# Optimization experiments

Hardware: AMD Instinct MI355X
Metric: run time of the kernel (lower is better)

## Reference

```python
import jax, jax.numpy as jnp
import numpy as np

N_VOX = 200000   # active voxels
K = 27           # 3x3x3 kernel offsets
P = 100000       # rulebook pairs per kernel offset
C_IN = 64
C_OUT = 64
BN_EPS = 1e-5


def setup_inputs() -> dict:
    key = jax.random.key(0)
    k1, k2, k3, k4, k5 = jax.random.split(key, 5)
    features = jax.random.normal(k1, (N_VOX, C_IN), dtype=jnp.float32)
    weight = jax.random.normal(k2, (K, C_IN, C_OUT), dtype=jnp.float32) * 0.05
    bias = jax.random.normal(k3, (C_OUT,), dtype=jnp.float32) * 0.05
    gamma = jnp.ones((C_OUT,), dtype=jnp.float32)
    beta = jnp.zeros((C_OUT,), dtype=jnp.float32)
    in_idx = jax.random.randint(k4, (K, P), 0, N_VOX, dtype=jnp.int32)
    out_idx = jax.random.randint(k5, (K, P), 0, N_VOX, dtype=jnp.int32)
    return {"features": features, "weight": weight, "bias": bias,
            "gamma": gamma, "beta": beta, "in_idx": in_idx, "out_idx": out_idx}


def reference(features, weight, bias, gamma, beta, in_idx, out_idx):
    # --- sparse submanifold conv: gather -> per-offset GEMM -> scatter-add ---
    gathered = features[in_idx]                         # [K, P, C_in]
    partial = jnp.einsum('kpc,kcd->kpd', gathered, weight)  # [K, P, C_out]
    out = jnp.zeros((N_VOX, C_OUT), dtype=features.dtype)
    out = out.at[out_idx.reshape(-1)].add(partial.reshape(-1, C_OUT))
    out = out + bias                                    # conv bias
    # --- BatchNorm1d (training mode: batch stats, biased variance) ---
    mean = jnp.mean(out, axis=0)
    var = jnp.mean(jnp.square(out - mean), axis=0)
    normed = (out - mean) * jax.lax.rsqrt(var + BN_EPS) * gamma + beta
    # --- ReLU ---
    return jnp.maximum(normed, 0.0)
```

## Files before the change

kernel.cpp:

```cpp
#include <hip/hip_runtime.h>
#include <hip/hip_bf16.h>

#define N_VOX 200000
#define KOFF 27
#define PPK 100000
#define C 64
#define BN_EPS 1e-5f

typedef __bf16 bf16x8 __attribute__((ext_vector_type(8)));
typedef __bf16 bf16x4 __attribute__((ext_vector_type(4)));
typedef float f32x4 __attribute__((ext_vector_type(4)));

__global__ __launch_bounds__(256)
void convert_features(const float* __restrict__ f, __bf16* __restrict__ fb)
{
    const size_t total4 = (size_t)N_VOX * C / 4;
    const size_t i = (size_t)blockIdx.x * blockDim.x + threadIdx.x;
    if (i >= total4) return;
    const float4 v = ((const float4*)f)[i];
    bf16x4 o;
    o.x = (__bf16)v.x; o.y = (__bf16)v.y; o.z = (__bf16)v.z; o.w = (__bf16)v.w;
    ((bf16x4*)fb)[i] = o;
}

__global__ __launch_bounds__(256)
void convert_weight(const float* __restrict__ w, __bf16* __restrict__ wt)
{
    const int k = blockIdx.x;
    const float* W = w + (size_t)k * C * C;
    __bf16* Wt = wt + (size_t)k * C * C;
    for (int idx = threadIdx.x; idx < C * C; idx += 256) {
        const int ci = idx >> 6, co = idx & 63;
        Wt[co * C + ci] = (__bf16)W[idx];
    }
}

__global__ __launch_bounds__(256)
void conv_mfma(const __bf16* __restrict__ featb, const __bf16* __restrict__ wtb,
               const int* __restrict__ in_idx, const int* __restrict__ out_idx,
               float* __restrict__ out)
{
    constexpr int TP = 256;
    constexpr int STRIDE = 72;
    __shared__ __bf16 sA[TP * STRIDE];
    __shared__ int s_out[TP];

    const int k = blockIdx.y;
    const int tile_base = blockIdx.x * TP;
    const int t = threadIdx.x;
    const int lane = t & 63;
    const int wave = t >> 6;
    const int m16 = lane & 15;
    const int quad = lane >> 4;

    const __bf16* Wt = wtb + (size_t)k * C * C;
    bf16x8 bfrag[4][2];
#pragma unroll
    for (int nt = 0; nt < 4; ++nt)
#pragma unroll
        for (int kc = 0; kc < 2; ++kc)
            bfrag[nt][kc] = *(const bf16x8*)(Wt + (nt * 16 + m16) * C + kc * 32 + quad * 8);

    {
        const int pair = tile_base + t;
        s_out[t] = (pair < PPK) ? out_idx[(size_t)k * PPK + pair] : 0;
    }

    const int c8 = t & 7;
    const int r0 = t >> 3;
#pragma unroll
    for (int it = 0; it < 8; ++it) {
        const int r = r0 + it * 32;
        const int pair = tile_base + r;
        const int row = (pair < PPK) ? in_idx[(size_t)k * PPK + pair] : 0;
        const float4 v = *(const float4*)(featb + (size_t)row * C + c8 * 8);
        *(float4*)(sA + r * STRIDE + c8 * 8) = v;
    }
    __syncthreads();

    f32x4 acc[4][4] = {};
    const int mbase = wave * 64;
#pragma unroll
    for (int kc = 0; kc < 2; ++kc) {
        bf16x8 afrag[4];
#pragma unroll
        for (int mt = 0; mt < 4; ++mt)
            afrag[mt] = *(const bf16x8*)(sA + (mbase + mt * 16 + m16) * STRIDE + kc * 32 + quad * 8);
#pragma unroll
        for (int nt = 0; nt < 4; ++nt)
#pragma unroll
            for (int mt = 0; mt < 4; ++mt)
                acc[mt][nt] = __builtin_amdgcn_mfma_f32_16x16x32_bf16(
                    afrag[mt], bfrag[nt][kc], acc[mt][nt], 0, 0, 0);
    }

#pragma unroll
    for (int mt = 0; mt < 4; ++mt) {
#pragma unroll
        for (int reg = 0; reg < 4; ++reg) {
            const int r = mbase + mt * 16 + quad * 4 + reg;
            const int pair = tile_base + r;
            if (pair < PPK) {
                const int o = s_out[r];
                float* orow = out + (size_t)o * C + m16;
#pragma unroll
                for (int nt = 0; nt < 4; ++nt)
                    unsafeAtomicAdd(orow + nt * 16, acc[mt][nt][reg]);
            }
        }
    }
}

__global__ __launch_bounds__(256)
void stats_kernel(const float* __restrict__ out,
                  float* __restrict__ stats,
                  int rows_per_block)
{
    __shared__ float ssum[256];
    __shared__ float ssq[256];
    const int c   = threadIdx.x & 63;
    const int sub = threadIdx.x >> 6;
    const int row0 = blockIdx.x * rows_per_block;
    const int row1 = min(row0 + rows_per_block, N_VOX);
    float s = 0.f, q = 0.f;
    for (int r = row0 + sub; r < row1; r += 4) {
        const float v = out[(size_t)r * C + c];
        s += v;
        q += v * v;
    }
    ssum[threadIdx.x] = s;
    ssq[threadIdx.x]  = q;
    __syncthreads();
    if (sub == 0) {
        s = ssum[c] + ssum[64 + c] + ssum[128 + c] + ssum[192 + c];
        q = ssq[c]  + ssq[64 + c]  + ssq[128 + c]  + ssq[192 + c];
        unsafeAtomicAdd(&stats[c], s);
        unsafeAtomicAdd(&stats[64 + c], q);
    }
}

__global__ void finalize_params(const float* __restrict__ stats,
                                const float* __restrict__ gamma,
                                const float* __restrict__ beta,
                                float* __restrict__ ss)
{
    const int c = threadIdx.x;
    const float inv_n = 1.0f / (float)N_VOX;
    const float mean  = stats[c] * inv_n;
    const float var   = stats[64 + c] * inv_n - mean * mean;
    const float scale = rsqrtf(var + BN_EPS) * gamma[c];
    ss[c]      = scale;
    ss[64 + c] = beta[c] - mean * scale;
}

__global__ __launch_bounds__(256)
void norm_kernel(float* __restrict__ out, const float* __restrict__ ss)
{
    const size_t total4 = (size_t)N_VOX * C / 4;
    const size_t idx = (size_t)blockIdx.x * blockDim.x + threadIdx.x;
    if (idx >= total4) return;
    const int c4 = (int)(idx & 15);
    float4 v = ((const float4*)out)[idx];
    const float4 sc = ((const float4*)ss)[c4];
    const float4 sh = ((const float4*)(ss + 64))[c4];
    v.x = fmaxf(v.x * sc.x + sh.x, 0.f);
    v.y = fmaxf(v.y * sc.y + sh.y, 0.f);
    v.z = fmaxf(v.z * sc.z + sh.z, 0.f);
    v.w = fmaxf(v.w * sc.w + sh.w, 0.f);
    ((float4*)out)[idx] = v;
}

extern "C" void kernel_launch(void* const* d_in, const int* in_sizes, int n_in,
                              void* d_out, int out_size, void* d_ws, size_t ws_size,
                              hipStream_t stream)
{
    const float* features = (const float*)d_in[0];
    const float* weight   = (const float*)d_in[1];
    const float* gamma    = (const float*)d_in[3];
    const float* beta     = (const float*)d_in[4];
    const int*   in_idx   = (const int*)d_in[5];
    const int*   out_idx  = (const int*)d_in[6];
    float* out = (float*)d_out;

    __bf16* featb = (__bf16*)d_ws;
    __bf16* wtb   = featb + (size_t)N_VOX * C;
    float*  stats = (float*)(wtb + (size_t)KOFF * C * C);
    float*  ss    = stats + 128;

    hipMemsetAsync(out, 0, (size_t)N_VOX * C * sizeof(float), stream);
    hipMemsetAsync(stats, 0, 128 * sizeof(float), stream);

    const size_t total4 = (size_t)N_VOX * C / 4;
    convert_features<<<(int)((total4 + 255) / 256), 256, 0, stream>>>(features, featb);
    convert_weight<<<KOFF, 256, 0, stream>>>(weight, wtb);

    dim3 cgrid((PPK + 255) / 256, KOFF);
    conv_mfma<<<cgrid, 256, 0, stream>>>(featb, wtb, in_idx, out_idx, out);

    const int rpb = (N_VOX + 511) / 512;
    stats_kernel<<<512, 256, 0, stream>>>(out, stats, rpb);

    finalize_params<<<1, 64, 0, stream>>>(stats, gamma, beta, ss);

    norm_kernel<<<(int)((total4 + 255) / 256), 256, 0, stream>>>(out, ss);
}
```

Baseline: 735.5 us.

## Replace float atomic scatter with counting-sort bucketed partials and segmented reduction

Builds a per-output-voxel histogram and prefix scan, then the conv kernel writes each pair's bf16 partial row into a slot grouped by destination voxel instead of doing float atomics into the output. A reduce kernel then sums each voxel's contiguous segment, writes the output and accumulates the BN statistics in the same pass. This removes the output memset, the 27×100k×64 scattered float atomics and the separate stats pass. In exchange it adds several small kernels, about 345 MB of bf16 partial traffic, and rounds partials to bf16 before summation. It falls back to the atomic path when the workspace is too small.

After: 736.2 us. Within noise of the previous version (+0.1%).

```diff
diff --git a/kernel.cpp b/kernel.cpp
--- a/kernel.cpp
+++ b/kernel.cpp
@@ -4,6 +4,7 @@
 #define N_VOX 200000
 #define KOFF 27
 #define PPK 100000
+#define NPAIRS (KOFF * PPK)
 #define C 64
 #define BN_EPS 1e-5f
 
@@ -36,14 +37,84 @@
 }
 
 __global__ __launch_bounds__(256)
-void conv_mfma(const __bf16* __restrict__ featb, const __bf16* __restrict__ wtb,
-               const int* __restrict__ in_idx, const int* __restrict__ out_idx,
-               float* __restrict__ out)
+void hist_kernel(const int* __restrict__ out_idx, int* __restrict__ cnt)
+{
+    const int i = blockIdx.x * 256 + threadIdx.x;
+    if (i < NPAIRS) atomicAdd(&cnt[out_idx[i]], 1);
+}
+
+__global__ __launch_bounds__(256)
+void scan_block_sums(const int* __restrict__ cnt, int* __restrict__ bsum)
+{
+    __shared__ int s[256];
+    const int t = threadIdx.x;
+    const int i0 = blockIdx.x * 1024 + t * 4;
+    int v = 0;
+#pragma unroll
+    for (int j = 0; j < 4; ++j) { const int i = i0 + j; if (i < N_VOX) v += cnt[i]; }
+    s[t] = v;
+    __syncthreads();
+    for (int d = 128; d > 0; d >>= 1) {
+        if (t < d) s[t] += s[t + d];
+        __syncthreads();
+    }
+    if (t == 0) bsum[blockIdx.x] = s[0];
+}
+
+__global__ __launch_bounds__(256)
+void scan_base(const int* __restrict__ bsum, int* __restrict__ bbase, int nblk)
+{
+    __shared__ int s[256];
+    const int t = threadIdx.x;
+    const int v = (t < nblk) ? bsum[t] : 0;
+    s[t] = v;
+    for (int d = 1; d < 256; d <<= 1) {
+        __syncthreads();
+        const int x = (t >= d) ? s[t - d] : 0;
+        __syncthreads();
+        s[t] += x;
+    }
+    if (t < nblk) bbase[t] = s[t] - v;
+}
+
+__global__ __launch_bounds__(256)
+void scan_write(const int* __restrict__ cnt, const int* __restrict__ bbase,
+                int* __restrict__ offs, int* __restrict__ cursor)
+{
+    __shared__ int s[256];
+    const int t = threadIdx.x;
+    const int i0 = blockIdx.x * 1024 + t * 4;
+    int v[4]; int local = 0;
+#pragma unroll
+    for (int j = 0; j < 4; ++j) {
+        const int i = i0 + j;
+        v[j] = (i < N_VOX) ? cnt[i] : 0;
+        local += v[j];
+    }
+    s[t] = local;
+    for (int d = 1; d < 256; d <<= 1) {
+        __syncthreads();
+        const int x = (t >= d) ? s[t - d] : 0;
+        __syncthreads();
+        s[t] += x;
+    }
+    int run = s[t] - local + bbase[blockIdx.x];
+#pragma unroll
+    for (int j = 0; j < 4; ++j) {
+        const int i = i0 + j;
+        if (i < N_VOX) { offs[i] = run; cursor[i] = run; run += v[j]; }
+    }
+}
+
+__global__ __launch_bounds__(256)
+void conv_mfma_sorted(const __bf16* __restrict__ featb, const __bf16* __restrict__ wtb,
+                      const int* __restrict__ in_idx, const int* __restrict__ out_idx,
+                      int* __restrict__ cursor, __bf16* __restrict__ partial)
 {
     constexpr int TP = 256;
     constexpr int STRIDE = 72;
     __shared__ __bf16 sA[TP * STRIDE];
-    __shared__ int s_out[TP];
+    __shared__ int s_dest[TP];
 
     const int k = blockIdx.y;
     const int tile_base = blockIdx.x * TP;
@@ -63,7 +134,10 @@
 
     {
         const int pair = tile_base + t;
-        s_out[t] = (pair < PPK) ? out_idx[(size_t)k * PPK + pair] : 0;
+        if (pair < PPK) {
+            const int ov = out_idx[(size_t)k * PPK + pair];
+            s_dest[t] = atomicAdd(&cursor[ov], 1);
+        }
     }
 
     const int c8 = t & 7;
@@ -93,47 +167,160 @@
                 acc[mt][nt] = __builtin_amdgcn_mfma_f32_16x16x32_bf16(
                     afrag[mt], bfrag[nt][kc], acc[mt][nt], 0, 0, 0);
     }
-
-#pragma unroll
-    for (int mt = 0; mt < 4; ++mt) {
+    __syncthreads();
+
+#pragma unroll
+    for (int mt = 0; mt < 4; ++mt)
+#pragma unroll
+        for (int reg = 0; reg < 4; ++reg) {
+            const int r = mbase + mt * 16 + quad * 4 + reg;
+#pragma unroll
+            for (int nt = 0; nt < 4; ++nt)
+                sA[r * STRIDE + nt * 16 + m16] = (__bf16)acc[mt][nt][reg];
+        }
+    __syncthreads();
+
+    const int hw = t >> 5;
+    const int l2 = t & 31;
+    for (int r = hw; r < TP; r += 8) {
+        const int pair = tile_base + r;
+        if (pair < PPK) {
+            const unsigned v = *(const unsigned*)((const char*)sA + (size_t)r * STRIDE * 2 + l2 * 4);
+            *(unsigned*)((char*)partial + (size_t)s_dest[r] * 128 + l2 * 4) = v;
+        }
+    }
+}
+
+__global__ __launch_bounds__(256)
+void reduce_stats(const __bf16* __restrict__ partial, const int* __restrict__ offs,
+                  float* __restrict__ out, float* __restrict__ stats)
+{
+    __shared__ float ssum[256];
+    __shared__ float ssq[256];
+    const int t = threadIdx.x;
+    const int lane = t & 63;
+    const int wave = t >> 6;
+    const int wglobal = blockIdx.x * 4 + wave;
+    const int nw = gridDim.x * 4;
+    const unsigned short* P = (const unsigned short*)partial;
+    float s = 0.f, q = 0.f;
+    for (int v = wglobal; v < N_VOX; v += nw) {
+        const int b = offs[v];
+        const int e = (v == N_VOX - 1) ? NPAIRS : offs[v + 1];
+        float a0 = 0.f, a1 = 0.f;
+        int i = b;
+        for (; i + 1 < e; i += 2) {
+            const unsigned u0 = P[(size_t)i * 64 + lane];
+            const unsigned u1 = P[(size_t)(i + 1) * 64 + lane];
+            a0 += __uint_as_float(u0 << 16);
+            a1 += __uint_as_float(u1 << 16);
+        }
+        if (i < e) a0 += __uint_as_float((unsigned)P[(size_t)i * 64 + lane] << 16);
+        const float a = a0 + a1;
+        out[(size_t)v * 64 + lane] = a;
+        s += a;
+        q += a * a;
+    }
+    ssum[t] = s;
+    ssq[t] = q;
+    __syncthreads();
+    if (wave == 0) {
+        s = ssum[lane] + ssum[64 + lane] + ssum[128 + lane] + ssum[192 + lane];
+        q = ssq[lane] + ssq[64 + lane] + ssq[128 + lane] + ssq[192 + lane];
+        unsafeAtomicAdd(&stats[lane], s);
+        unsafeAtomicAdd(&stats[64 + lane], q);
+    }
+}
+
+__global__ __launch_bounds__(256)
+void conv_mfma_atomic(const __bf16* __restrict__ featb, const __bf16* __restrict__ wtb,
+                      const int* __restrict__ in_idx, const int* __restrict__ out_idx,
+                      float* __restrict__ out)
+{
+    constexpr int TP = 256;
+    constexpr int STRIDE = 72;
+    __shared__ __bf16 sA[TP * STRIDE];
+    __shared__ int s_out[TP];
+    const int k = blockIdx.y;
+    const int tile_base = blockIdx.x * TP;
+    const int t = threadIdx.x;
+    const int lane = t & 63;
+    const int wave = t >> 6;
+    const int m16 = lane & 15;
+    const int quad = lane >> 4;
+    const __bf16* Wt = wtb + (size_t)k * C * C;
+    bf16x8 bfrag[4][2];
+#pragma unroll
+    for (int nt = 0; nt < 4; ++nt)
+#pragma unroll
+        for (int kc = 0; kc < 2; ++kc)
+            bfrag[nt][kc] = *(const bf16x8*)(Wt + (nt * 16 + m16) * C + kc * 32 + quad * 8);
+    {
+        const int pair = tile_base + t;
+        s_out[t] = (pair < PPK) ? out_idx[(size_t)k * PPK + pair] : 0;
+    }
+    const int c8 = t & 7;
+    const int r0 = t >> 3;
+#pragma unroll
+    for (int it = 0; it < 8; ++it) {
+        const int r = r0 + it * 32;
+        const int pair = tile_base + r;
+        const int row = (pair < PPK) ? in_idx[(size_t)k * PPK + pair] : 0;
+        const float4 v = *(const float4*)(featb + (size_t)row * C + c8 * 8);
+        *(float4*)(sA + r * STRIDE + c8 * 8) = v;
+    }
+    __syncthreads();
+    f32x4 acc[4][4] = {};
+    const int mbase = wave * 64;
+#pragma unroll
+    for (int kc = 0; kc < 2; ++kc) {
+        bf16x8 afrag[4];
+#pragma unroll
+        for (int mt = 0; mt < 4; ++mt)
+            afrag[mt] = *(const bf16x8*)(sA + (mbase + mt * 16 + m16) * STRIDE + kc * 32 + quad * 8);
+#pragma unroll
+        for (int nt = 0; nt < 4; ++nt)
+#pragma unroll
+            for (int mt = 0; mt < 4; ++mt)
+                acc[mt][nt] = __builtin_amdgcn_mfma_f32_16x16x32_bf16(
+                    afrag[mt], bfrag[nt][kc], acc[mt][nt], 0, 0, 0);
+    }
+#pragma unroll
+    for (int mt = 0; mt < 4; ++mt)
 #pragma unroll
         for (int reg = 0; reg < 4; ++reg) {
             const int r = mbase + mt * 16 + quad * 4 + reg;
             const int pair = tile_base + r;
             if (pair < PPK) {
-                const int o = s_out[r];
-                float* orow = out + (size_t)o * C + m16;
+                float* orow = out + (size_t)s_out[r] * C + m16;
 #pragma unroll
                 for (int nt = 0; nt < 4; ++nt)
                     unsafeAtomicAdd(orow + nt * 16, acc[mt][nt][reg]);
             }
         }
-    }
-}
-
-__global__ __launch_bounds__(256)
-void stats_kernel(const float* __restrict__ out,
-                  float* __restrict__ stats,
+}
+
+__global__ __launch_bounds__(256)
+void stats_kernel(const float* __restrict__ out, float* __restrict__ stats,
                   int rows_per_block)
 {
     __shared__ float ssum[256];
     __shared__ float ssq[256];
-    const int c   = threadIdx.x & 63;
+    const int c = threadIdx.x & 63;
     const int sub = threadIdx.x >> 6;
     const int row0 = blockIdx.x * rows_per_block;
     const int row1 = min(row0 + rows_per_block, N_VOX);
     float s = 0.f, q = 0.f;
     for (int r = row0 + sub; r < row1; r += 4) {
         const float v = out[(size_t)r * C + c];
-        s += v;
-        q += v * v;
+        s += v; q += v * v;
     }
     ssum[threadIdx.x] = s;
-    ssq[threadIdx.x]  = q;
+    ssq[threadIdx.x] = q;
     __syncthreads();
     if (sub == 0) {
         s = ssum[c] + ssum[64 + c] + ssum[128 + c] + ssum[192 + c];
-        q = ssq[c]  + ssq[64 + c]  + ssq[128 + c]  + ssq[192 + c];
+        q = ssq[c] + ssq[64 + c] + ssq[128 + c] + ssq[192 + c];
         unsafeAtomicAdd(&stats[c], s);
         unsafeAtomicAdd(&stats[64 + c], q);
     }
@@ -146,10 +333,10 @@
 {
     const int c = threadIdx.x;
     const float inv_n = 1.0f / (float)N_VOX;
-    const float mean  = stats[c] * inv_n;
-    const float var   = stats[64 + c] * inv_n - mean * mean;
+    const float mean = stats[c] * inv_n;
+    const float var = stats[64 + c] * inv_n - mean * mean;
     const float scale = rsqrtf(var + BN_EPS) * gamma[c];
-    ss[c]      = scale;
+    ss[c] = scale;
     ss[64 + c] = beta[c] - mean * scale;
 }
 
@@ -182,25 +369,53 @@
     const int*   out_idx  = (const int*)d_in[6];
     float* out = (float*)d_out;
 
-    __bf16* featb = (__bf16*)d_ws;
-    __bf16* wtb   = featb + (size_t)N_VOX * C;
-    float*  stats = (float*)(wtb + (size_t)KOFF * C * C);
-    float*  ss    = stats + 128;
-
-    hipMemsetAsync(out, 0, (size_t)N_VOX * C * sizeof(float), stream);
+    char* base = (char*)d_ws;
+    size_t cur = 0;
+    auto alloc = [&](size_t bytes) -> char* {
+        char* p = base + cur;
+        cur = (cur + bytes + 255) & ~(size_t)255;
+        return p;
+    };
+    __bf16* featb  = (__bf16*)alloc((size_t)N_VOX * C * 2);
+    __bf16* wtb    = (__bf16*)alloc((size_t)KOFF * C * C * 2);
+    float*  stats  = (float*)alloc(128 * 4);
+    float*  ss     = (float*)alloc(128 * 4);
+    int*    cnt    = (int*)alloc((size_t)N_VOX * 4);
+    int*    offs   = (int*)alloc((size_t)N_VOX * 4);
+    int*    cursor = (int*)alloc((size_t)N_VOX * 4);
+    int*    bsum   = (int*)alloc(256 * 4);
+    int*    bbase  = (int*)alloc(256 * 4);
+    size_t fast_head = cur;
+    __bf16* partial = (__bf16*)alloc((size_t)NPAIRS * C * 2);
+    const bool fast = (ws_size >= cur);
+
+    const size_t total4 = (size_t)N_VOX * C / 4;
+    const int nb_elem = (int)((total4 + 255) / 256);
+
     hipMemsetAsync(stats, 0, 128 * sizeof(float), stream);
-
-    const size_t total4 = (size_t)N_VOX * C / 4;
-    convert_features<<<(int)((total4 + 255) / 256), 256, 0, stream>>>(features, featb);
+    convert_features<<<nb_elem, 256, 0, stream>>>(features, featb);
     convert_weight<<<KOFF, 256, 0, stream>>>(weight, wtb);
 
     dim3 cgrid((PPK + 255) / 256, KOFF);
-    conv_mfma<<<cgrid, 256, 0, stream>>>(featb, wtb, in_idx, out_idx, out);
-
-    const int rpb = (N_VOX + 511) / 512;
-    stats_kernel<<<512, 256, 0, stream>>>(out, stats, rpb);
+
+    if (fast) {
+        (void)fast_head;
+        hipMemsetAsync(cnt, 0, (size_t)N_VOX * 4, stream);
+        hist_kernel<<<(NPAIRS + 255) / 256, 256, 0, stream>>>(out_idx, cnt);
+        const int nscan = (N_VOX + 1023) / 1024;
+        scan_block_sums<<<nscan, 256, 0, stream>>>(cnt, bsum);
+        scan_base<<<1, 256, 0, stream>>>(bsum, bbase, nscan);
+        scan_write<<<nscan, 256, 0, stream>>>(cnt, bbase, offs, cursor);
+        conv_mfma_sorted<<<cgrid, 256, 0, stream>>>(featb, wtb, in_idx, out_idx,
+                                                    cursor, partial);
+        reduce_stats<<<512, 256, 0, stream>>>(partial, offs, out, stats);
+    } else {
+        hipMemsetAsync(out, 0, (size_t)N_VOX * C * sizeof(float), stream);
+        conv_mfma_atomic<<<cgrid, 256, 0, stream>>>(featb, wtb, in_idx, out_idx, out);
+        const int rpb = (N_VOX + 511) / 512;
+        stats_kernel<<<512, 256, 0, stream>>>(out, stats, rpb);
+    }
 
     finalize_params<<<1, 64, 0, stream>>>(stats, gamma, beta, ss);
-
-    norm_kernel<<<(int)((total4 + 255) / 256), 256, 0, stream>>>(out, ss);
-}
+    norm_kernel<<<nb_elem, 256, 0, stream>>>(out, ss);
+}
```

## Replace atomic scatter-add conv with output-owner bucketed gather GEMM

Applied to the files above, without the earlier changes.

Builds a per-(output voxel, offset) bucket table with two slots, plus a spill list, using an atomic scatter pass over the rulebook. An owner-computes kernel then accumulates each output row in registers with MFMA and writes it once, and a spill kernel atomically adds the overflow pairs. This removes the per-element float atomics to the output and the output memset. In exchange it adds the 21.6MB counter memset, the bucket build with integer atomics, and many MFMAs wasted on sparse, mostly-empty slots. BN stats now use per-block partials reduced in finalize instead of atomics.

Result: slower. 1.048 ms (+42.5%).

```diff
diff --git a/kernel.cpp b/kernel.cpp
--- a/kernel.cpp
+++ b/kernel.cpp
@@ -4,8 +4,12 @@
 #define N_VOX 200000
 #define KOFF 27
 #define PPK 100000
+#define NPAIRS (KOFF * PPK)
 #define C 64
 #define BN_EPS 1e-5f
+#define CAP 2
+#define SPILL_CAP (1 << 19)
+#define STAT_BLOCKS 512
 
 typedef __bf16 bf16x8 __attribute__((ext_vector_type(8)));
 typedef __bf16 bf16x4 __attribute__((ext_vector_type(4)));
@@ -36,120 +40,157 @@
 }
 
 __global__ __launch_bounds__(256)
-void conv_mfma(const __bf16* __restrict__ featb, const __bf16* __restrict__ wtb,
-               const int* __restrict__ in_idx, const int* __restrict__ out_idx,
+void scatter_slots(const int* __restrict__ in_idx, const int* __restrict__ out_idx,
+                   int* __restrict__ cnt2, int* __restrict__ slot,
+                   int* __restrict__ spill_n, int2* __restrict__ spill)
+{
+    const int i = blockIdx.x * 256 + threadIdx.x;
+    if (i >= NPAIRS) return;
+    const int v = out_idx[i];
+    const int k = i / PPK;
+    const int key = v * KOFF + k;
+    const int j = atomicAdd(&cnt2[key], 1);
+    const int in = in_idx[i];
+    if (j < CAP) {
+        slot[key * CAP + j] = in;
+    } else {
+        const int p = atomicAdd(spill_n, 1);
+        if (p < SPILL_CAP) spill[p] = make_int2(in, key);
+    }
+}
+
+__global__ __launch_bounds__(256)
+void gemm_owner(const __bf16* __restrict__ featb, const __bf16* __restrict__ wtb,
+                const int* __restrict__ cnt2, const int* __restrict__ slot,
+                float* __restrict__ out)
+{
+    const int t = threadIdx.x;
+    const int lane = t & 63, wave = t >> 6;
+    const int m16 = lane & 15, quad = lane >> 4;
+    const int vbase = blockIdx.x * 64 + wave * 16;
+    const int myv = vbase + m16;
+
+    f32x4 acc[4] = {};
+
+    int key = myv * KOFF;
+    int c_n = min(cnt2[key], CAP);
+    int2 sl_n = ((const int2*)slot)[key];
+
+    for (int k = 0; k < KOFF; ++k) {
+        const int cc = c_n;
+        const int2 s = sl_n;
+        if (k + 1 < KOFF) {
+            c_n = min(cnt2[key + 1], CAP);
+            sl_n = ((const int2*)slot)[key + 1];
+        }
+        ++key;
+
+        int D = cc;
+        D = max(D, __shfl_xor(D, 1, 16));
+        D = max(D, __shfl_xor(D, 2, 16));
+        D = max(D, __shfl_xor(D, 4, 16));
+        D = max(D, __shfl_xor(D, 8, 16));
+        if (D == 0) continue;
+
+        const __bf16* W = wtb + (size_t)k * C * C;
+        bf16x8 bf[4][2];
+#pragma unroll
+        for (int nt = 0; nt < 4; ++nt) {
+            bf[nt][0] = *(const bf16x8*)(W + (nt * 16 + m16) * C + quad * 8);
+            bf[nt][1] = *(const bf16x8*)(W + (nt * 16 + m16) * C + 32 + quad * 8);
+        }
+
+        for (int j = 0; j < D; ++j) {
+            const int fi = (j == 0) ? s.x : s.y;
+            bf16x8 a0 = {}, a1 = {};
+            if (j < cc) {
+                const __bf16* fp = featb + (size_t)fi * C + quad * 8;
+                a0 = *(const bf16x8*)fp;
+                a1 = *(const bf16x8*)(fp + 32);
+            }
+#pragma unroll
+            for (int nt = 0; nt < 4; ++nt) {
+                acc[nt] = __builtin_amdgcn_mfma_f32_16x16x32_bf16(a0, bf[nt][0], acc[nt], 0, 0, 0);
+                acc[nt] = __builtin_amdgcn_mfma_f32_16x16x32_bf16(a1, bf[nt][1], acc[nt], 0, 0, 0);
+            }
+        }
+    }
+
+#pragma unroll
+    for (int nt = 0; nt < 4; ++nt)
+#pragma unroll
+        for (int reg = 0; reg < 4; ++reg) {
+            const int vm = vbase + quad * 4 + reg;
+            out[(size_t)vm * C + nt * 16 + m16] = acc[nt][reg];
+        }
+}
+
+__global__ __launch_bounds__(256)
+void spill_fix(const __bf16* __restrict__ featb, const __bf16* __restrict__ wtb,
+               const int2* __restrict__ spill, const int* __restrict__ spill_n,
                float* __restrict__ out)
 {
-    constexpr int TP = 256;
-    constexpr int STRIDE = 72;
-    __shared__ __bf16 sA[TP * STRIDE];
-    __shared__ int s_out[TP];
-
-    const int k = blockIdx.y;
-    const int tile_base = blockIdx.x * TP;
-    const int t = threadIdx.x;
-    const int lane = t & 63;
-    const int wave = t >> 6;
-    const int m16 = lane & 15;
-    const int quad = lane >> 4;
-
-    const __bf16* Wt = wtb + (size_t)k * C * C;
-    bf16x8 bfrag[4][2];
-#pragma unroll
-    for (int nt = 0; nt < 4; ++nt)
-#pragma unroll
-        for (int kc = 0; kc < 2; ++kc)
-            bfrag[nt][kc] = *(const bf16x8*)(Wt + (nt * 16 + m16) * C + kc * 32 + quad * 8);
-
-    {
-        const int pair = tile_base + t;
-        s_out[t] = (pair < PPK) ? out_idx[(size_t)k * PPK + pair] : 0;
-    }
-
-    const int c8 = t & 7;
-    const int r0 = t >> 3;
-#pragma unroll
-    for (int it = 0; it < 8; ++it) {
-        const int r = r0 + it * 32;
-        const int pair = tile_base + r;
-        const int row = (pair < PPK) ? in_idx[(size_t)k * PPK + pair] : 0;
-        const float4 v = *(const float4*)(featb + (size_t)row * C + c8 * 8);
-        *(float4*)(sA + r * STRIDE + c8 * 8) = v;
-    }
-    __syncthreads();
-
-    f32x4 acc[4][4] = {};
-    const int mbase = wave * 64;
-#pragma unroll
-    for (int kc = 0; kc < 2; ++kc) {
-        bf16x8 afrag[4];
-#pragma unroll
-        for (int mt = 0; mt < 4; ++mt)
-            afrag[mt] = *(const bf16x8*)(sA + (mbase + mt * 16 + m16) * STRIDE + kc * 32 + quad * 8);
-#pragma unroll
-        for (int nt = 0; nt < 4; ++nt)
-#pragma unroll
-            for (int mt = 0; mt < 4; ++mt)
-                acc[mt][nt] = __builtin_amdgcn_mfma_f32_16x16x32_bf16(
-                    afrag[mt], bfrag[nt][kc], acc[mt][nt], 0, 0, 0);
-    }
-
-#pragma unroll
-    for (int mt = 0; mt < 4; ++mt) {
-#pragma unroll
-        for (int reg = 0; reg < 4; ++reg) {
-            const int r = mbase + mt * 16 + quad * 4 + reg;
-            const int pair = tile_base + r;
-            if (pair < PPK) {
-                const int o = s_out[r];
-                float* orow = out + (size_t)o * C + m16;
-#pragma unroll
-                for (int nt = 0; nt < 4; ++nt)
-                    unsafeAtomicAdd(orow + nt * 16, acc[mt][nt][reg]);
-            }
-        }
-    }
-}
-
-__global__ __launch_bounds__(256)
-void stats_kernel(const float* __restrict__ out,
-                  float* __restrict__ stats,
-                  int rows_per_block)
+    const int lane = threadIdx.x & 63, wave = threadIdx.x >> 6;
+    const int n = min(*spill_n, SPILL_CAP);
+    for (int p = blockIdx.x * 4 + wave; p < n; p += gridDim.x * 4) {
+        const int2 e = spill[p];
+        const int key = e.y;
+        const int v = key / KOFF;
+        const int k = key - v * KOFF;
+        const __bf16* fr = featb + (size_t)e.x * C;
+        const __bf16* wr = wtb + (size_t)k * C * C + lane * C;
+        float a0 = 0.f, a1 = 0.f;
+#pragma unroll
+        for (int i = 0; i < C; i += 2) {
+            a0 += (float)fr[i] * (float)wr[i];
+            a1 += (float)fr[i + 1] * (float)wr[i + 1];
+        }
+        unsafeAtomicAdd(&out[(size_t)v * C + lane], a0 + a1);
+    }
+}
+
+__global__ __launch_bounds__(256)
+void stats_partial(const float* __restrict__ out, float* __restrict__ bst,
+                   int rows_per_block)
 {
     __shared__ float ssum[256];
     __shared__ float ssq[256];
-    const int c   = threadIdx.x & 63;
+    const int c = threadIdx.x & 63;
     const int sub = threadIdx.x >> 6;
     const int row0 = blockIdx.x * rows_per_block;
     const int row1 = min(row0 + rows_per_block, N_VOX);
     float s = 0.f, q = 0.f;
     for (int r = row0 + sub; r < row1; r += 4) {
         const float v = out[(size_t)r * C + c];
-        s += v;
-        q += v * v;
+        s += v; q += v * v;
     }
     ssum[threadIdx.x] = s;
-    ssq[threadIdx.x]  = q;
+    ssq[threadIdx.x] = q;
     __syncthreads();
     if (sub == 0) {
         s = ssum[c] + ssum[64 + c] + ssum[128 + c] + ssum[192 + c];
-        q = ssq[c]  + ssq[64 + c]  + ssq[128 + c]  + ssq[192 + c];
-        unsafeAtomicAdd(&stats[c], s);
-        unsafeAtomicAdd(&stats[64 + c], q);
-    }
-}
-
-__global__ void finalize_params(const float* __restrict__ stats,
+        q = ssq[c] + ssq[64 + c] + ssq[128 + c] + ssq[192 + c];
+        bst[blockIdx.x * 128 + c] = s;
+        bst[blockIdx.x * 128 + 64 + c] = q;
+    }
+}
+
+__global__ void finalize_params(const float* __restrict__ bst,
                                 const float* __restrict__ gamma,
                                 const float* __restrict__ beta,
                                 float* __restrict__ ss)
 {
     const int c = threadIdx.x;
+    float s = 0.f, q = 0.f;
+    for (int b = 0; b < STAT_BLOCKS; ++b) {
+        s += bst[b * 128 + c];
+        q += bst[b * 128 + 64 + c];
+    }
     const float inv_n = 1.0f / (float)N_VOX;
-    const float mean  = stats[c] * inv_n;
-    const float var   = stats[64 + c] * inv_n - mean * mean;
+    const float mean = s * inv_n;
+    const float var = q * inv_n - mean * mean;
     const float scale = rsqrtf(var + BN_EPS) * gamma[c];
-    ss[c]      = scale;
+    ss[c] = scale;
     ss[64 + c] = beta[c] - mean * scale;
 }
 
@@ -170,6 +211,74 @@
     ((float4*)out)[idx] = v;
 }
 
+__global__ __launch_bounds__(256)
+void conv_mfma_atomic(const __bf16* __restrict__ featb, const __bf16* __restrict__ wtb,
+                      const int* __restrict__ in_idx, const int* __restrict__ out_idx,
+                      float* __restrict__ out)
+{
+    constexpr int TP = 256;
+    constexpr int STRIDE = 72;
+    __shared__ __bf16 sA[TP * STRIDE];
+    __shared__ int s_out[TP];
+    const int k = blockIdx.y;
+    const int tile_base = blockIdx.x * TP;
+    const int t = threadIdx.x;
+    const int lane = t & 63;
+    const int wave = t >> 6;
+    const int m16 = lane & 15;
+    const int quad = lane >> 4;
+    const __bf16* Wt = wtb + (size_t)k * C * C;
+    bf16x8 bfrag[4][2];
+#pragma unroll
+    for (int nt = 0; nt < 4; ++nt)
+#pragma unroll
+        for (int kc = 0; kc < 2; ++kc)
+            bfrag[nt][kc] = *(const bf16x8*)(Wt + (nt * 16 + m16) * C + kc * 32 + quad * 8);
+    {
+        const int pair = tile_base + t;
+        s_out[t] = (pair < PPK) ? out_idx[(size_t)k * PPK + pair] : 0;
+    }
+    const int c8 = t & 7;
+    const int r0 = t >> 3;
+#pragma unroll
+    for (int it = 0; it < 8; ++it) {
+        const int r = r0 + it * 32;
+        const int pair = tile_base + r;
+        const int row = (pair < PPK) ? in_idx[(size_t)k * PPK + pair] : 0;
+        const float4 v = *(const float4*)(featb + (size_t)row * C + c8 * 8);
+        *(float4*)(sA + r * STRIDE + c8 * 8) = v;
+    }
+    __syncthreads();
+    f32x4 acc[4][4] = {};
+    const int mbase = wave * 64;
+#pragma unroll
+    for (int kc = 0; kc < 2; ++kc) {
+        bf16x8 afrag[4];
+#pragma unroll
+        for (int mt = 0; mt < 4; ++mt)
+            afrag[mt] = *(const bf16x8*)(sA + (mbase + mt * 16 + m16) * STRIDE + kc * 32 + quad * 8);
+#pragma unroll
+        for (int nt = 0; nt < 4; ++nt)
+#pragma unroll
+            for (int mt = 0; mt < 4; ++mt)
+                acc[mt][nt] = __builtin_amdgcn_mfma_f32_16x16x32_bf16(
+                    afrag[mt], bfrag[nt][kc], acc[mt][nt], 0, 0, 0);
+    }
+#pragma unroll
+    for (int mt = 0; mt < 4; ++mt)
+#pragma unroll
+        for (int reg = 0; reg < 4; ++reg) {
+            const int r = mbase + mt * 16 + quad * 4 + reg;
+            const int pair = tile_base + r;
+            if (pair < PPK) {
+                float* orow = out + (size_t)s_out[r] * C + m16;
+#pragma unroll
+                for (int nt = 0; nt < 4; ++nt)
+                    unsafeAtomicAdd(orow + nt * 16, acc[mt][nt][reg]);
+            }
+        }
+}
+
 extern "C" void kernel_launch(void* const* d_in, const int* in_sizes, int n_in,
                               void* d_out, int out_size, void* d_ws, size_t ws_size,
                               hipStream_t stream)
@@ -182,25 +291,48 @@
     const int*   out_idx  = (const int*)d_in[6];
     float* out = (float*)d_out;
 
-    __bf16* featb = (__bf16*)d_ws;
-    __bf16* wtb   = featb + (size_t)N_VOX * C;
-    float*  stats = (float*)(wtb + (size_t)KOFF * C * C);
-    float*  ss    = stats + 128;
-
-    hipMemsetAsync(out, 0, (size_t)N_VOX * C * sizeof(float), stream);
-    hipMemsetAsync(stats, 0, 128 * sizeof(float), stream);
+    char* base = (char*)d_ws;
+    size_t cur = 0;
+    auto alloc = [&](size_t bytes) -> char* {
+        char* p = base + cur;
+        cur = (cur + bytes + 255) & ~(size_t)255;
+        return p;
+    };
+    __bf16* featb   = (__bf16*)alloc((size_t)N_VOX * C * 2);
+    __bf16* wtb     = (__bf16*)alloc((size_t)KOFF * C * C * 2);
+    float*  ss      = (float*)alloc(128 * 4);
+    float*  bst     = (float*)alloc((size_t)STAT_BLOCKS * 128 * 4);
+    int*    cnt2    = (int*)alloc((size_t)N_VOX * KOFF * 4);
+    int*    slot    = (int*)alloc((size_t)N_VOX * KOFF * CAP * 4);
+    int*    spill_n = (int*)alloc(256);
+    int2*   spill   = (int2*)alloc((size_t)SPILL_CAP * 8);
+    const bool fast = (ws_size >= cur);
 
     const size_t total4 = (size_t)N_VOX * C / 4;
-    convert_features<<<(int)((total4 + 255) / 256), 256, 0, stream>>>(features, featb);
+    const int nb_elem = (int)((total4 + 255) / 256);
+    const int nb_pair = (NPAIRS + 255) / 256;
+
+    convert_features<<<nb_elem, 256, 0, stream>>>(features, featb);
     convert_weight<<<KOFF, 256, 0, stream>>>(weight, wtb);
 
-    dim3 cgrid((PPK + 255) / 256, KOFF);
-    conv_mfma<<<cgrid, 256, 0, stream>>>(featb, wtb, in_idx, out_idx, out);
-
-    const int rpb = (N_VOX + 511) / 512;
-    stats_kernel<<<512, 256, 0, stream>>>(out, stats, rpb);
-
-    finalize_params<<<1, 64, 0, stream>>>(stats, gamma, beta, ss);
-
-    norm_kernel<<<(int)((total4 + 255) / 256), 256, 0, stream>>>(out, ss);
-}
+    if (fast) {
+        hipMemsetAsync(cnt2, 0, (size_t)N_VOX * KOFF * 4, stream);
+        hipMemsetAsync(spill_n, 0, 4, stream);
+
+        scatter_slots<<<nb_pair, 256, 0, stream>>>(in_idx, out_idx, cnt2, slot,
+                                                   spill_n, spill);
+
+        gemm_owner<<<N_VOX / 64, 256, 0, stream>>>(featb, wtb, cnt2, slot, out);
+
+        spill_fix<<<2048, 256, 0, stream>>>(featb, wtb, spill, spill_n, out);
+    } else {
+        hipMemsetAsync(out, 0, (size_t)N_VOX * C * sizeof(float), stream);
+        dim3 cgrid((PPK + 255) / 256, KOFF);
+        conv_mfma_atomic<<<cgrid, 256, 0, stream>>>(featb, wtb, in_idx, out_idx, out);
+    }
+
+    const int rpb = (N_VOX + STAT_BLOCKS - 1) / STAT_BLOCKS;
+    stats_partial<<<STAT_BLOCKS, 256, 0, stream>>>(out, bst, rpb);
+    finalize_params<<<1, 64, 0, stream>>>(bst, gamma, beta, ss);
+    norm_kernel<<<nb_elem, 256, 0, stream>>>(out, ss);
+}
```
